# Performance work log

Measured on AMD Instinct MI355X. Metric: run time of the kernel, lower is better.

Reference implementation:

```python
import jax, jax.numpy as jnp
import numpy as np

R = 4
EPS = 0.1


def _box(x, r=R):
    # Depthwise (2r+1)x(2r+1) mean filter with 'SAME' zero padding, faithful to
    # F.conv2d(x, box_kernel, groups=C, padding='same').
    c = x.shape[1]
    k = 2 * r + 1
    kernel = jnp.full((c, 1, k, k), 1.0 / (k * k), dtype=x.dtype)  # OIHW, groups=C
    return jax.lax.conv_general_dilated(
        x, kernel, window_strides=(1, 1), padding='SAME',
        dimension_numbers=('NCHW', 'OIHW', 'NCHW'), feature_group_count=c)


def setup_inputs() -> dict:
    key = jax.random.key(0)
    k1, k2 = jax.random.split(key)
    x = jax.random.uniform(k1, (8, 3, 768, 768), dtype=jnp.float32)
    y = jax.random.uniform(k2, (8, 3, 768, 768), dtype=jnp.float32)
    return {"x": x, "y": y}


def reference(x, y):
    n, c, h, w = x.shape
    # N: box filter of an all-ones [1,1,H,W] image (edge-normalization counts)
    N = _box(jnp.ones((1, 1, h, w), dtype=x.dtype))
    mean_x = _box(x) / N
    mean_y = _box(y) / N
    cov_xy = _box(x * y) / N - mean_x * mean_y
    var_x = _box(x * x) / N - mean_x * mean_x
    A = cov_xy / (var_x + EPS)
    b = mean_y - A * mean_x
    mean_A = _box(A) / N
    mean_b = _box(b) / N
    return mean_A * x + mean_b
```

## Files before the change

### kernel.cpp

```cpp
#include <hip/hip_runtime.h>

#define H 768
#define W 768
#define SW 256
#define RW 272
#define ABWID 264
#define ROWS 64
#define STEPS 80
#define RADIUS 4

__global__ __launch_bounds__(256, 4) void gf_stream(
    const float* __restrict__ xg, const float* __restrict__ yg,
    float* __restrict__ outg)
{
    __shared__ float2 xyrow[RW];
    __shared__ float  xring[9][RW];
    __shared__ float2 abrow[ABWID];
    __shared__ float4 tring[9][8];

    const int t     = threadIdx.x;
    const int strip = blockIdx.x;
    const int band  = blockIdx.y;
    const int plane = blockIdx.z;
    const int base  = strip * SW;
    const int R0    = band * ROWS;

    const float* xp = xg + (size_t)plane * (H * W);
    const float* yp = yg + (size_t)plane * (H * W);
    float*       op = outg + (size_t)plane * (H * W);

    const int  a_abs   = base + t - 4;
    const bool a_colok = (a_abs >= 0) && (a_abs < W);
    const float invCwA = a_colok
        ? 1.0f / (float)(min(a_abs + RADIUS, W - 1) - max(a_abs - RADIUS, 0) + 1) : 0.f;
    const int  a2_abs   = base + 252 + t;
    const bool a2_colok = (t < 8) && (a2_abs < W);
    const float invCwA2 = a2_colok
        ? 1.0f / (float)(min(a2_abs + RADIUS, W - 1) - max(a2_abs - RADIUS, 0) + 1) : 0.f;
    const int   c_abs  = base + t;
    const float invCwO = 1.0f / (float)(min(c_abs + RADIUS, W - 1) - max(c_abs - RADIUS, 0) + 1);
    const int  lc1   = base + t - 8;
    const bool lc1ok = (lc1 >= 0) && (lc1 < W);
    const int  lc2   = base + 248 + t;
    const bool lc2ok = (t < 16) && (lc2 < W);

    float hx[9], hy[9], hxy[9], hxx[9];
    float hA9[9], hB9[9];
#pragma unroll
    for (int i = 0; i < 9; ++i) { hx[i] = hy[i] = hxy[i] = hxx[i] = 0.f; hA9[i] = hB9[i] = 0.f; }
    float vx = 0.f, vy = 0.f, vxy = 0.f, vxx = 0.f;
    float v2x = 0.f, v2y = 0.f, v2xy = 0.f, v2xx = 0.f;
    float vA = 0.f, vB = 0.f;

    if (t < 72) ((float4*)tring)[t] = make_float4(0.f, 0.f, 0.f, 0.f);

    float gx, gy, gx2, gy2;
    {
        int gr = R0 - 8;
        bool rok = (gr >= 0);
        const float* xr = xp + gr * W;
        const float* yr = yp + gr * W;
        gx  = (rok && lc1ok) ? xr[lc1] : 0.f;
        gy  = (rok && lc1ok) ? yr[lc1] : 0.f;
        gx2 = (rok && lc2ok) ? xr[lc2] : 0.f;
        gy2 = (rok && lc2ok) ? yr[lc2] : 0.f;
    }

    for (int so = 0; so < STEPS; so += 9) {
#pragma unroll
        for (int oo = 0; oo < 9; ++oo) {
            const int s = so + oo;
            if (s < STEPS) {
                const int r = R0 - 16 + s;

                __syncthreads();

                const int wr = (r + 8) % 9;
                xyrow[t] = make_float2(gx, gy);
                xring[wr][t] = gx;
                if (t < 16) {
                    xyrow[256 + t] = make_float2(gx2, gy2);
                    xring[wr][256 + t] = gx2;
                }
                {
                    int gr = r + 9;
                    bool rok = (gr >= 0) && (gr < H);
                    const float* xr = xp + gr * W;
                    const float* yr = yp + gr * W;
                    gx  = (rok && lc1ok) ? xr[lc1] : 0.f;
                    gy  = (rok && lc1ok) ? yr[lc1] : 0.f;
                    gx2 = (rok && lc2ok) ? xr[lc2] : 0.f;
                    gy2 = (rok && lc2ok) ? yr[lc2] : 0.f;
                }

                __syncthreads();

                float nx = 0.f, ny = 0.f, nxy = 0.f, nxx = 0.f;
#pragma unroll
                for (int d = 0; d < 9; ++d) {
                    float2 v = xyrow[t + d];
                    nx += v.x; ny += v.y; nxy += v.x * v.y; nxx += v.x * v.x;
                }
                vx  += nx  - hx[oo];  hx[oo]  = nx;
                vy  += ny  - hy[oo];  hy[oo]  = ny;
                vxy += nxy - hxy[oo]; hxy[oo] = nxy;
                vxx += nxx - hxx[oo]; hxx[oo] = nxx;

                const int ra = r + 4;
                const bool rowok = (s >= 8) && (ra >= 0) && (ra < H);
                const float invChA = rowok
                    ? 1.0f / (float)(min(ra + RADIUS, H - 1) - max(ra - RADIUS, 0) + 1) : 0.f;
                float Aout = 0.f, Bout = 0.f;
                if (rowok && a_colok) {
                    float invN = invChA * invCwA;
                    float mx = vx * invN, my = vy * invN;
                    float cov = vxy * invN - mx * my;
                    float vr  = vxx * invN - mx * mx;
                    Aout = cov / (vr + 0.1f);
                    Bout = my - Aout * mx;
                }
                abrow[t] = make_float2(Aout, Bout);

                if (t < 8) {
                    float ex = 0.f, ey = 0.f, exy = 0.f, exx = 0.f;
#pragma unroll
                    for (int d = 0; d < 9; ++d) {
                        float2 v = xyrow[256 + t + d];
                        ex += v.x; ey += v.y; exy += v.x * v.y; exx += v.x * v.x;
                    }
                    float4 old = tring[oo][t];
                    v2x += ex - old.x; v2y += ey - old.y;
                    v2xy += exy - old.z; v2xx += exx - old.w;
                    tring[oo][t] = make_float4(ex, ey, exy, exx);
                    float A2 = 0.f, B2 = 0.f;
                    if (rowok && a2_colok) {
                        float invN = invChA * invCwA2;
                        float mx = v2x * invN, my = v2y * invN;
                        float cov = v2xy * invN - mx * my;
                        float vr  = v2xx * invN - mx * mx;
                        A2 = cov / (vr + 0.1f);
                        B2 = my - A2 * mx;
                    }
                    abrow[256 + t] = make_float2(A2, B2);
                }

                __syncthreads();

                float hAn = 0.f, hBn = 0.f;
#pragma unroll
                for (int d = 0; d < 9; ++d) {
                    float2 v = abrow[t + d];
                    hAn += v.x; hBn += v.y;
                }
                vA += hAn - hA9[oo]; hA9[oo] = hAn;
                vB += hBn - hB9[oo]; hB9[oo] = hBn;

                if (s >= 16) {
                    float xo = xring[r % 9][t + 8];
                    const float invChO =
                        1.0f / (float)(min(r + RADIUS, H - 1) - max(r - RADIUS, 0) + 1);
                    float invN2 = invChO * invCwO;
                    op[r * W + c_abs] = (vA * invN2) * xo + (vB * invN2);
                }
            }
        }
    }
}

extern "C" void kernel_launch(void* const* d_in, const int* in_sizes, int n_in,
                              void* d_out, int out_size, void* d_ws, size_t ws_size,
                              hipStream_t stream) {
    const float* x = (const float*)d_in[0];
    const float* y = (const float*)d_in[1];
    float* out = (float*)d_out;

    dim3 grid(W / SW, H / ROWS, 24);
    dim3 block(256);
    hipLaunchKernelGGL(gf_stream, grid, block, 0, stream, x, y, out);
}
```

Before: 107.5 us.

## Process two rows per step with double-buffered LDS to cut barriers

Restructures the streaming loop to handle two rows per iteration, with double-buffered row and A/B buffers in shared memory. This drops from three barriers per row to one barrier per two rows. The x value for the output is now reloaded from global memory instead of an LDS ring, and the division is replaced by a hardware reciprocal approximation. The trade-offs are more registers, extra global reads, and slightly lower precision from rcp.

```diff
diff --git a/kernel.cpp b/kernel.cpp
--- a/kernel.cpp
+++ b/kernel.cpp
@@ -4,26 +4,23 @@
 #define W 768
 #define SW 256
 #define RW 272
-#define ABWID 264
+#define ABW 264
 #define ROWS 64
-#define STEPS 80
+#define NSTEP 40
 #define RADIUS 4
 
-__global__ __launch_bounds__(256, 4) void gf_stream(
+__global__ __launch_bounds__(256, 4) void gf_stream2(
     const float* __restrict__ xg, const float* __restrict__ yg,
     float* __restrict__ outg)
 {
-    __shared__ float2 xyrow[RW];
-    __shared__ float  xring[9][RW];
-    __shared__ float2 abrow[ABWID];
+    __shared__ float2 xybuf[2][2][RW];
+    __shared__ float2 abbuf[2][2][ABW];
     __shared__ float4 tring[9][8];
 
     const int t     = threadIdx.x;
-    const int strip = blockIdx.x;
-    const int band  = blockIdx.y;
+    const int base  = blockIdx.x * SW;
+    const int R0    = blockIdx.y * ROWS;
     const int plane = blockIdx.z;
-    const int base  = strip * SW;
-    const int R0    = band * ROWS;
 
     const float* xp = xg + (size_t)plane * (H * W);
     const float* yp = yg + (size_t)plane * (H * W);
@@ -47,120 +44,195 @@
     float hx[9], hy[9], hxy[9], hxx[9];
     float hA9[9], hB9[9];
 #pragma unroll
-    for (int i = 0; i < 9; ++i) { hx[i] = hy[i] = hxy[i] = hxx[i] = 0.f; hA9[i] = hB9[i] = 0.f; }
-    float vx = 0.f, vy = 0.f, vxy = 0.f, vxx = 0.f;
-    float v2x = 0.f, v2y = 0.f, v2xy = 0.f, v2xx = 0.f;
-    float vA = 0.f, vB = 0.f;
-
-    if (t < 72) ((float4*)tring)[t] = make_float4(0.f, 0.f, 0.f, 0.f);
-
-    float gx, gy, gx2, gy2;
+    for (int i = 0; i < 9; ++i) { hx[i]=hy[i]=hxy[i]=hxx[i]=0.f; hA9[i]=hB9[i]=0.f; }
+    float vx=0.f, vy=0.f, vxy=0.f, vxx=0.f;
+    float v2x=0.f, v2y=0.f, v2xy=0.f, v2xx=0.f;
+    float vA=0.f, vB=0.f;
+
+    if (t < 72) ((float4*)tring)[t] = make_float4(0.f,0.f,0.f,0.f);
+
     {
-        int gr = R0 - 8;
-        bool rok = (gr >= 0);
-        const float* xr = xp + gr * W;
-        const float* yr = yp + gr * W;
-        gx  = (rok && lc1ok) ? xr[lc1] : 0.f;
-        gy  = (rok && lc1ok) ? yr[lc1] : 0.f;
-        gx2 = (rok && lc2ok) ? xr[lc2] : 0.f;
-        gy2 = (rok && lc2ok) ? yr[lc2] : 0.f;
+        int g0 = R0 - 8, g1 = R0 - 7;
+        bool k0 = (g0 >= 0), k1 = (g1 >= 0);
+        const float *x0 = xp + g0 * W, *y0 = yp + g0 * W;
+        const float *x1 = xp + g1 * W, *y1 = yp + g1 * W;
+        float a, b;
+        a = (k0 && lc1ok) ? x0[lc1] : 0.f;  b = (k0 && lc1ok) ? y0[lc1] : 0.f;
+        xybuf[0][0][t] = make_float2(a, b);
+        a = (k1 && lc1ok) ? x1[lc1] : 0.f;  b = (k1 && lc1ok) ? y1[lc1] : 0.f;
+        xybuf[0][1][t] = make_float2(a, b);
+        if (t < 16) {
+            a = (k0 && lc2ok) ? x0[lc2] : 0.f;  b = (k0 && lc2ok) ? y0[lc2] : 0.f;
+            xybuf[0][0][256 + t] = make_float2(a, b);
+            a = (k1 && lc2ok) ? x1[lc2] : 0.f;  b = (k1 && lc2ok) ? y1[lc2] : 0.f;
+            xybuf[0][1][256 + t] = make_float2(a, b);
+        }
     }
-
-    for (int so = 0; so < STEPS; so += 9) {
-#pragma unroll
-        for (int oo = 0; oo < 9; ++oo) {
-            const int s = so + oo;
-            if (s < STEPS) {
-                const int r = R0 - 16 + s;
+    float p0x, p0y, p0x2, p0y2, p1x, p1y, p1x2, p1y2;
+    {
+        int g0 = R0 - 6, g1 = R0 - 5;
+        bool k0 = (g0 >= 0), k1 = (g1 >= 0);
+        const float *x0 = xp + g0 * W, *y0 = yp + g0 * W;
+        const float *x1 = xp + g1 * W, *y1 = yp + g1 * W;
+        p0x  = (k0 && lc1ok) ? x0[lc1] : 0.f;  p0y  = (k0 && lc1ok) ? y0[lc1] : 0.f;
+        p1x  = (k1 && lc1ok) ? x1[lc1] : 0.f;  p1y  = (k1 && lc1ok) ? y1[lc1] : 0.f;
+        p0x2 = (k0 && lc2ok) ? x0[lc2] : 0.f;  p0y2 = (k0 && lc2ok) ? y0[lc2] : 0.f;
+        p1x2 = (k1 && lc2ok) ? x1[lc2] : 0.f;  p1y2 = (k1 && lc2ok) ? y1[lc2] : 0.f;
+    }
+    __syncthreads();
+
+    for (int S0 = 0; S0 < NSTEP; S0 += 9) {
+#pragma unroll
+        for (int u = 0; u < 9; ++u) {
+            const int S = S0 + u;
+            if (S < NSTEP) {
+                const int r0  = R0 - 16 + 2 * S;
+                const int cur = S & 1, nxt = cur ^ 1;
+
+                xybuf[nxt][0][t] = make_float2(p0x, p0y);
+                xybuf[nxt][1][t] = make_float2(p1x, p1y);
+                if (t < 16) {
+                    xybuf[nxt][0][256 + t] = make_float2(p0x2, p0y2);
+                    xybuf[nxt][1][256 + t] = make_float2(p1x2, p1y2);
+                }
+                {
+                    int g0 = r0 + 12, g1 = r0 + 13;
+                    bool k0 = (g0 >= 0) && (g0 < H);
+                    bool k1 = (g1 >= 0) && (g1 < H);
+                    const float *x0 = xp + g0 * W, *y0 = yp + g0 * W;
+                    const float *x1 = xp + g1 * W, *y1 = yp + g1 * W;
+                    p0x  = (k0 && lc1ok) ? x0[lc1] : 0.f;  p0y  = (k0 && lc1ok) ? y0[lc1] : 0.f;
+                    p1x  = (k1 && lc1ok) ? x1[lc1] : 0.f;  p1y  = (k1 && lc1ok) ? y1[lc1] : 0.f;
+                    p0x2 = (k0 && lc2ok) ? x0[lc2] : 0.f;  p0y2 = (k0 && lc2ok) ? y0[lc2] : 0.f;
+                    p1x2 = (k1 && lc2ok) ? x1[lc2] : 0.f;  p1y2 = (k1 && lc2ok) ? y1[lc2] : 0.f;
+                }
+                float xq0 = (r0 >= 0)     ? xp[r0 * W + c_abs]       : 0.f;
+                float xq1 = (r0 + 1 >= 0) ? xp[(r0 + 1) * W + c_abs] : 0.f;
+
+                {
+                    const int sl = (2 * u) % 9;
+                    float nx=0.f, ny=0.f, nxy=0.f, nxx=0.f;
+#pragma unroll
+                    for (int d = 0; d < 9; ++d) {
+                        float2 v = xybuf[cur][0][t + d];
+                        nx += v.x; ny += v.y; nxy += v.x * v.y; nxx += v.x * v.x;
+                    }
+                    vx  += nx  - hx[sl];  hx[sl]  = nx;
+                    vy  += ny  - hy[sl];  hy[sl]  = ny;
+                    vxy += nxy - hxy[sl]; hxy[sl] = nxy;
+                    vxx += nxx - hxx[sl]; hxx[sl] = nxx;
+
+                    const int ra = r0 + 4;
+                    const bool rowok = (S >= 4) && (ra >= 0) && (ra < H);
+                    float Aout = 0.f, Bout = 0.f;
+                    if (rowok && a_colok) {
+                        const float invCh = 1.0f /
+                            (float)(min(ra + RADIUS, H - 1) - max(ra - RADIUS, 0) + 1);
+                        float invN = invCh * invCwA;
+                        float mx = vx * invN, my = vy * invN;
+                        float cov = vxy * invN - mx * my;
+                        float vr  = vxx * invN - mx * mx;
+                        float Ai = cov * __builtin_amdgcn_rcpf(vr + 0.1f);
+                        Aout = Ai; Bout = my - Ai * mx;
+                    }
+                    abbuf[cur][0][t] = make_float2(Aout, Bout);
+                }
+                {
+                    const int sl = (2 * u + 1) % 9;
+                    float nx=0.f, ny=0.f, nxy=0.f, nxx=0.f;
+#pragma unroll
+                    for (int d = 0; d < 9; ++d) {
+                        float2 v = xybuf[cur][1][t + d];
+                        nx += v.x; ny += v.y; nxy += v.x * v.y; nxx += v.x * v.x;
+                    }
+                    vx  += nx  - hx[sl];  hx[sl]  = nx;
+                    vy  += ny  - hy[sl];  hy[sl]  = ny;
+                    vxy += nxy - hxy[sl]; hxy[sl] = nxy;
+                    vxx += nxx - hxx[sl]; hxx[sl] = nxx;
+
+                    const int ra = r0 + 5;
+                    const bool rowok = (S >= 4) && (ra >= 0) && (ra < H);
+                    float Aout = 0.f, Bout = 0.f;
+                    if (rowok && a_colok) {
+                        const float invCh = 1.0f /
+                            (float)(min(ra + RADIUS, H - 1) - max(ra - RADIUS, 0) + 1);
+                        float invN = invCh * invCwA;
+                        float mx = vx * invN, my = vy * invN;
+                        float cov = vxy * invN - mx * my;
+                        float vr  = vxx * invN - mx * mx;
+                        float Ai = cov * __builtin_amdgcn_rcpf(vr + 0.1f);
+                        Aout = Ai; Bout = my - Ai * mx;
+                    }
+                    abbuf[cur][1][t] = make_float2(Aout, Bout);
+                }
+                if (t < 8) {
+#pragma unroll
+                    for (int j = 0; j < 2; ++j) {
+                        const int sl = (2 * u + j) % 9;
+                        float ex=0.f, ey=0.f, exy=0.f, exx=0.f;
+#pragma unroll
+                        for (int d = 0; d < 9; ++d) {
+                            float2 v = xybuf[cur][j][256 + t + d];
+                            ex += v.x; ey += v.y; exy += v.x * v.y; exx += v.x * v.x;
+                        }
+                        float4 old = tring[sl][t];
+                        v2x += ex - old.x; v2y += ey - old.y;
+                        v2xy += exy - old.z; v2xx += exx - old.w;
+                        tring[sl][t] = make_float4(ex, ey, exy, exx);
+
+                        const int ra = r0 + 4 + j;
+                        const bool rowok = (S >= 4) && (ra >= 0) && (ra < H);
+                        float A2 = 0.f, B2 = 0.f;
+                        if (rowok && a2_colok) {
+                            const float invCh = 1.0f /
+                                (float)(min(ra + RADIUS, H - 1) - max(ra - RADIUS, 0) + 1);
+                            float invN = invCh * invCwA2;
+                            float mx = v2x * invN, my = v2y * invN;
+                            float cov = v2xy * invN - mx * my;
+                            float vr  = v2xx * invN - mx * mx;
+                            float Ai = cov * __builtin_amdgcn_rcpf(vr + 0.1f);
+                            A2 = Ai; B2 = my - Ai * mx;
+                        }
+                        abbuf[cur][j][256 + t] = make_float2(A2, B2);
+                    }
+                }
 
                 __syncthreads();
 
-                const int wr = (r + 8) % 9;
-                xyrow[t] = make_float2(gx, gy);
-                xring[wr][t] = gx;
-                if (t < 16) {
-                    xyrow[256 + t] = make_float2(gx2, gy2);
-                    xring[wr][256 + t] = gx2;
-                }
-                {
-                    int gr = r + 9;
-                    bool rok = (gr >= 0) && (gr < H);
-                    const float* xr = xp + gr * W;
-                    const float* yr = yp + gr * W;
-                    gx  = (rok && lc1ok) ? xr[lc1] : 0.f;
-                    gy  = (rok && lc1ok) ? yr[lc1] : 0.f;
-                    gx2 = (rok && lc2ok) ? xr[lc2] : 0.f;
-                    gy2 = (rok && lc2ok) ? yr[lc2] : 0.f;
-                }
-
-                __syncthreads();
-
-                float nx = 0.f, ny = 0.f, nxy = 0.f, nxx = 0.f;
-#pragma unroll
-                for (int d = 0; d < 9; ++d) {
-                    float2 v = xyrow[t + d];
-                    nx += v.x; ny += v.y; nxy += v.x * v.y; nxx += v.x * v.x;
-                }
-                vx  += nx  - hx[oo];  hx[oo]  = nx;
-                vy  += ny  - hy[oo];  hy[oo]  = ny;
-                vxy += nxy - hxy[oo]; hxy[oo] = nxy;
-                vxx += nxx - hxx[oo]; hxx[oo] = nxx;
-
-                const int ra = r + 4;
-                const bool rowok = (s >= 8) && (ra >= 0) && (ra < H);
-                const float invChA = rowok
-                    ? 1.0f / (float)(min(ra + RADIUS, H - 1) - max(ra - RADIUS, 0) + 1) : 0.f;
-                float Aout = 0.f, Bout = 0.f;
-                if (rowok && a_colok) {
-                    float invN = invChA * invCwA;
-                    float mx = vx * invN, my = vy * invN;
-                    float cov = vxy * invN - mx * my;
-                    float vr  = vxx * invN - mx * mx;
-                    Aout = cov / (vr + 0.1f);
-                    Bout = my - Aout * mx;
-                }
-                abrow[t] = make_float2(Aout, Bout);
-
-                if (t < 8) {
-                    float ex = 0.f, ey = 0.f, exy = 0.f, exx = 0.f;
-#pragma unroll
-                    for (int d = 0; d < 9; ++d) {
-                        float2 v = xyrow[256 + t + d];
-                        ex += v.x; ey += v.y; exy += v.x * v.y; exx += v.x * v.x;
-                    }
-                    float4 old = tring[oo][t];
-                    v2x += ex - old.x; v2y += ey - old.y;
-                    v2xy += exy - old.z; v2xx += exx - old.w;
-                    tring[oo][t] = make_float4(ex, ey, exy, exx);
-                    float A2 = 0.f, B2 = 0.f;
-                    if (rowok && a2_colok) {
-                        float invN = invChA * invCwA2;
-                        float mx = v2x * invN, my = v2y * invN;
-                        float cov = v2xy * invN - mx * my;
-                        float vr  = v2xx * invN - mx * mx;
-                        A2 = cov / (vr + 0.1f);
-                        B2 = my - A2 * mx;
-                    }
-                    abrow[256 + t] = make_float2(A2, B2);
-                }
-
-                __syncthreads();
-
-                float hAn = 0.f, hBn = 0.f;
-#pragma unroll
-                for (int d = 0; d < 9; ++d) {
-                    float2 v = abrow[t + d];
-                    hAn += v.x; hBn += v.y;
-                }
-                vA += hAn - hA9[oo]; hA9[oo] = hAn;
-                vB += hBn - hB9[oo]; hB9[oo] = hBn;
-
-                if (s >= 16) {
-                    float xo = xring[r % 9][t + 8];
-                    const float invChO =
-                        1.0f / (float)(min(r + RADIUS, H - 1) - max(r - RADIUS, 0) + 1);
-                    float invN2 = invChO * invCwO;
-                    op[r * W + c_abs] = (vA * invN2) * xo + (vB * invN2);
+                {
+                    const int sl = (2 * u) % 9;
+                    float hA=0.f, hB=0.f;
+#pragma unroll
+                    for (int d = 0; d < 9; ++d) {
+                        float2 v = abbuf[cur][0][t + d];
+                        hA += v.x; hB += v.y;
+                    }
+                    vA += hA - hA9[sl]; hA9[sl] = hA;
+                    vB += hB - hB9[sl]; hB9[sl] = hB;
+                    if (S >= 8) {
+                        const float invCh = 1.0f /
+                            (float)(min(r0 + RADIUS, H - 1) - max(r0 - RADIUS, 0) + 1);
+                        float invN = invCh * invCwO;
+                        op[r0 * W + c_abs] = (vA * invN) * xq0 + (vB * invN);
+                    }
+                }
+                {
+                    const int sl = (2 * u + 1) % 9;
+                    float hA=0.f, hB=0.f;
+#pragma unroll
+                    for (int d = 0; d < 9; ++d) {
+                        float2 v = abbuf[cur][1][t + d];
+                        hA += v.x; hB += v.y;
+                    }
+                    vA += hA - hA9[sl]; hA9[sl] = hA;
+                    vB += hB - hB9[sl]; hB9[sl] = hB;
+                    if (S >= 8) {
+                        const int r = r0 + 1;
+                        const float invCh = 1.0f /
+                            (float)(min(r + RADIUS, H - 1) - max(r - RADIUS, 0) + 1);
+                        float invN = invCh * invCwO;
+                        op[r * W + c_abs] = (vA * invN) * xq1 + (vB * invN);
+                    }
                 }
             }
         }
@@ -176,5 +248,5 @@
 
     dim3 grid(W / SW, H / ROWS, 24);
     dim3 block(256);
-    hipLaunchKernelGGL(gf_stream, grid, block, 0, stream, x, y, out);
+    hipLaunchKernelGGL(gf_stream2, grid, block, 0, stream, x, y, out);
 }
```

Result: faster. 103.8 us (-3.4%).

## Double-buffer row stages to cut barriers to one per row, shrink row bands

Applied to the files above, without the earlier changes.

Double-buffers the xy row and AB row shared arrays so each streamed row needs one __syncthreads instead of three. Input loads are prefetched one extra row ahead, and the x ring grows to 11 slots to cover the longer lag. The band height drops from 64 to 48 rows, which gives more blocks but a higher share of warm-up rows (16 of 64 steps instead of 16 of 80). The divides become fast reciprocals, which slightly changes the precision of A.

```diff
diff --git a/kernel.cpp b/kernel.cpp
--- a/kernel.cpp
+++ b/kernel.cpp
@@ -4,26 +4,25 @@
 #define W 768
 #define SW 256
 #define RW 272
-#define ABWID 264
-#define ROWS 64
-#define STEPS 80
+#define ABW 264
+#define ROWS 48
+#define STEPS 64
+#define XR 11
 #define RADIUS 4
 
-__global__ __launch_bounds__(256, 4) void gf_stream(
+__global__ __launch_bounds__(256, 4) void gf_stream6(
     const float* __restrict__ xg, const float* __restrict__ yg,
     float* __restrict__ outg)
 {
-    __shared__ float2 xyrow[RW];
-    __shared__ float  xring[9][RW];
-    __shared__ float2 abrow[ABWID];
+    __shared__ float2 xybuf[2][RW];
+    __shared__ float2 abbuf[2][ABW];
+    __shared__ float  xring[XR][RW];
     __shared__ float4 tring[9][8];
 
     const int t     = threadIdx.x;
-    const int strip = blockIdx.x;
-    const int band  = blockIdx.y;
+    const int base  = blockIdx.x * SW;
+    const int R0    = blockIdx.y * ROWS;
     const int plane = blockIdx.z;
-    const int base  = strip * SW;
-    const int R0    = band * ROWS;
 
     const float* xp = xg + (size_t)plane * (H * W);
     const float* yp = yg + (size_t)plane * (H * W);
@@ -45,122 +44,132 @@
     const bool lc2ok = (t < 16) && (lc2 < W);
 
     float hx[9], hy[9], hxy[9], hxx[9];
-    float hA9[9], hB9[9];
+    float aA[9], aB[9];
 #pragma unroll
-    for (int i = 0; i < 9; ++i) { hx[i] = hy[i] = hxy[i] = hxx[i] = 0.f; hA9[i] = hB9[i] = 0.f; }
-    float vx = 0.f, vy = 0.f, vxy = 0.f, vxx = 0.f;
-    float v2x = 0.f, v2y = 0.f, v2xy = 0.f, v2xx = 0.f;
-    float vA = 0.f, vB = 0.f;
+    for (int i = 0; i < 9; ++i) { hx[i]=hy[i]=hxy[i]=hxx[i]=0.f; aA[i]=aB[i]=0.f; }
+    float vx=0.f, vy=0.f, vxy=0.f, vxx=0.f;
+    float v2x=0.f, v2y=0.f, v2xy=0.f, v2xx=0.f;
+    float vA=0.f, vB=0.f;
 
-    if (t < 72) ((float4*)tring)[t] = make_float4(0.f, 0.f, 0.f, 0.f);
+    if (t < 72) ((float4*)tring)[t] = make_float4(0.f,0.f,0.f,0.f);
 
-    float gx, gy, gx2, gy2;
     {
-        int gr = R0 - 8;
-        bool rok = (gr >= 0);
-        const float* xr = xp + gr * W;
-        const float* yr = yp + gr * W;
-        gx  = (rok && lc1ok) ? xr[lc1] : 0.f;
-        gy  = (rok && lc1ok) ? yr[lc1] : 0.f;
-        gx2 = (rok && lc2ok) ? xr[lc2] : 0.f;
-        gy2 = (rok && lc2ok) ? yr[lc2] : 0.f;
+        int g = R0 - 8;
+        bool k = (g >= 0);
+        const float *xr_ = xp + g * W, *yr_ = yp + g * W;
+        float a = (k && lc1ok) ? xr_[lc1] : 0.f;
+        float b = (k && lc1ok) ? yr_[lc1] : 0.f;
+        xybuf[0][t] = make_float2(a, b);
+        if (t < 16) {
+            float c = (k && lc2ok) ? xr_[lc2] : 0.f;
+            float d = (k && lc2ok) ? yr_[lc2] : 0.f;
+            xybuf[0][256 + t] = make_float2(c, d);
+        }
     }
+    float px_, py_, px2_, py2_;
+    {
+        int g = R0 - 7;
+        bool k = (g >= 0);
+        const float *xr_ = xp + g * W, *yr_ = yp + g * W;
+        px_  = (k && lc1ok) ? xr_[lc1] : 0.f;  py_  = (k && lc1ok) ? yr_[lc1] : 0.f;
+        px2_ = (k && lc2ok) ? xr_[lc2] : 0.f;  py2_ = (k && lc2ok) ? yr_[lc2] : 0.f;
+    }
+    __syncthreads();
 
-    for (int so = 0; so < STEPS; so += 9) {
+    for (int S0 = 0; S0 < STEPS; S0 += 9) {
 #pragma unroll
-        for (int oo = 0; oo < 9; ++oo) {
-            const int s = so + oo;
-            if (s < STEPS) {
-                const int r = R0 - 16 + s;
+        for (int u = 0; u < 9; ++u) {
+            const int S = S0 + u;
+            if (S < STEPS) {
+                const int r   = R0 - 16 + S;
+                const int cur = S & 1, nxt = cur ^ 1;
+                const int slw = (R0 + S + 15) % XR;
+                const int slr = (R0 + S + 6)  % XR;
 
-                __syncthreads();
-
-                const int wr = (r + 8) % 9;
-                xyrow[t] = make_float2(gx, gy);
-                xring[wr][t] = gx;
+                xybuf[nxt][t] = make_float2(px_, py_);
+                xring[slw][t] = px_;
                 if (t < 16) {
-                    xyrow[256 + t] = make_float2(gx2, gy2);
-                    xring[wr][256 + t] = gx2;
+                    xybuf[nxt][256 + t] = make_float2(px2_, py2_);
+                    xring[slw][256 + t] = px2_;
                 }
                 {
-                    int gr = r + 9;
-                    bool rok = (gr >= 0) && (gr < H);
-                    const float* xr = xp + gr * W;
-                    const float* yr = yp + gr * W;
-                    gx  = (rok && lc1ok) ? xr[lc1] : 0.f;
-                    gy  = (rok && lc1ok) ? yr[lc1] : 0.f;
-                    gx2 = (rok && lc2ok) ? xr[lc2] : 0.f;
-                    gy2 = (rok && lc2ok) ? yr[lc2] : 0.f;
+                    int g = r + 10;
+                    bool k = (g >= 0) && (g < H);
+                    const float *xr_ = xp + g * W, *yr_ = yp + g * W;
+                    px_  = (k && lc1ok) ? xr_[lc1] : 0.f;  py_  = (k && lc1ok) ? yr_[lc1] : 0.f;
+                    px2_ = (k && lc2ok) ? xr_[lc2] : 0.f;  py2_ = (k && lc2ok) ? yr_[lc2] : 0.f;
+                }
+
+                float nx=0.f, ny=0.f, nxy=0.f, nxx=0.f;
+#pragma unroll
+                for (int d = 0; d < 9; ++d) {
+                    float2 v = xybuf[cur][t + d];
+                    nx += v.x; ny += v.y; nxy += v.x * v.y; nxx += v.x * v.x;
+                }
+                vx  += nx  - hx[u];  hx[u]  = nx;
+                vy  += ny  - hy[u];  hy[u]  = ny;
+                vxy += nxy - hxy[u]; hxy[u] = nxy;
+                vxx += nxx - hxx[u]; hxx[u] = nxx;
+
+                const int ra = r + 4;
+                if (S >= 8) {
+                    float A0 = 0.f, B0 = 0.f;
+                    if (a_colok && ra >= 0 && ra < H) {
+                        const float invCh = 1.0f /
+                            (float)(min(ra + RADIUS, H - 1) - max(ra - RADIUS, 0) + 1);
+                        float invN = invCh * invCwA;
+                        float mx = vx * invN, my = vy * invN;
+                        float cov = vxy * invN - mx * my;
+                        float vr  = vxx * invN - mx * mx;
+                        A0 = cov * __builtin_amdgcn_rcpf(vr + 0.1f);
+                        B0 = my - A0 * mx;
+                    }
+                    abbuf[cur][t] = make_float2(A0, B0);
+                }
+                if (t < 8) {
+                    float ex=0.f, ey=0.f, exy=0.f, exx=0.f;
+#pragma unroll
+                    for (int d = 0; d < 9; ++d) {
+                        float2 v = xybuf[cur][256 + t + d];
+                        ex += v.x; ey += v.y; exy += v.x * v.y; exx += v.x * v.x;
+                    }
+                    float4 o = tring[u][t];
+                    v2x += ex - o.x; v2y += ey - o.y; v2xy += exy - o.z; v2xx += exx - o.w;
+                    tring[u][t] = make_float4(ex, ey, exy, exx);
+                    if (S >= 8) {
+                        float A2 = 0.f, B2 = 0.f;
+                        if (a2_colok && ra >= 0 && ra < H) {
+                            const float invCh = 1.0f /
+                                (float)(min(ra + RADIUS, H - 1) - max(ra - RADIUS, 0) + 1);
+                            float invN = invCh * invCwA2;
+                            float mx = v2x * invN, my = v2y * invN;
+                            float cov = v2xy * invN - mx * my;
+                            float vr  = v2xx * invN - mx * mx;
+                            A2 = cov * __builtin_amdgcn_rcpf(vr + 0.1f);
+                            B2 = my - A2 * mx;
+                        }
+                        abbuf[cur][256 + t] = make_float2(A2, B2);
+                    }
                 }
 
                 __syncthreads();
 
-                float nx = 0.f, ny = 0.f, nxy = 0.f, nxx = 0.f;
-#pragma unroll
-                for (int d = 0; d < 9; ++d) {
-                    float2 v = xyrow[t + d];
-                    nx += v.x; ny += v.y; nxy += v.x * v.y; nxx += v.x * v.x;
-                }
-                vx  += nx  - hx[oo];  hx[oo]  = nx;
-                vy  += ny  - hy[oo];  hy[oo]  = ny;
-                vxy += nxy - hxy[oo]; hxy[oo] = nxy;
-                vxx += nxx - hxx[oo]; hxx[oo] = nxx;
-
-                const int ra = r + 4;
-                const bool rowok = (s >= 8) && (ra >= 0) && (ra < H);
-                const float invChA = rowok
-                    ? 1.0f / (float)(min(ra + RADIUS, H - 1) - max(ra - RADIUS, 0) + 1) : 0.f;
-                float Aout = 0.f, Bout = 0.f;
-                if (rowok && a_colok) {
-                    float invN = invChA * invCwA;
-                    float mx = vx * invN, my = vy * invN;
-                    float cov = vxy * invN - mx * my;
-                    float vr  = vxx * invN - mx * mx;
-                    Aout = cov / (vr + 0.1f);
-                    Bout = my - Aout * mx;
-                }
-                abrow[t] = make_float2(Aout, Bout);
-
-                if (t < 8) {
-                    float ex = 0.f, ey = 0.f, exy = 0.f, exx = 0.f;
+                if (S >= 8) {
+                    float hA=0.f, hB=0.f;
 #pragma unroll
                     for (int d = 0; d < 9; ++d) {
-                        float2 v = xyrow[256 + t + d];
-                        ex += v.x; ey += v.y; exy += v.x * v.y; exx += v.x * v.x;
+                        float2 v = abbuf[cur][t + d];
+                        hA += v.x; hB += v.y;
                     }
-                    float4 old = tring[oo][t];
-                    v2x += ex - old.x; v2y += ey - old.y;
-                    v2xy += exy - old.z; v2xx += exx - old.w;
-                    tring[oo][t] = make_float4(ex, ey, exy, exx);
-                    float A2 = 0.f, B2 = 0.f;
-                    if (rowok && a2_colok) {
-                        float invN = invChA * invCwA2;
-                        float mx = v2x * invN, my = v2y * invN;
-                        float cov = v2xy * invN - mx * my;
-                        float vr  = v2xx * invN - mx * mx;
-                        A2 = cov / (vr + 0.1f);
-                        B2 = my - A2 * mx;
+                    vA += hA - aA[u]; aA[u] = hA;
+                    vB += hB - aB[u]; aB[u] = hB;
+                    if (S >= 16) {
+                        float xo = xring[slr][t + 8];
+                        const float invCh = 1.0f /
+                            (float)(min(r + RADIUS, H - 1) - max(r - RADIUS, 0) + 1);
+                        float invN = invCh * invCwO;
+                        op[r * W + c_abs] = (vA * invN) * xo + (vB * invN);
                     }
-                    abrow[256 + t] = make_float2(A2, B2);
-                }
-
-                __syncthreads();
-
-                float hAn = 0.f, hBn = 0.f;
-#pragma unroll
-                for (int d = 0; d < 9; ++d) {
-                    float2 v = abrow[t + d];
-                    hAn += v.x; hBn += v.y;
-                }
-                vA += hAn - hA9[oo]; hA9[oo] = hAn;
-                vB += hBn - hB9[oo]; hB9[oo] = hBn;
-
-                if (s >= 16) {
-                    float xo = xring[r % 9][t + 8];
-                    const float invChO =
-                        1.0f / (float)(min(r + RADIUS, H - 1) - max(r - RADIUS, 0) + 1);
-                    float invN2 = invChO * invCwO;
-                    op[r * W + c_abs] = (vA * invN2) * xo + (vB * invN2);
                 }
             }
         }
@@ -176,5 +185,5 @@
 
     dim3 grid(W / SW, H / ROWS, 24);
     dim3 block(256);
-    hipLaunchKernelGGL(gf_stream, grid, block, 0, stream, x, y, out);
+    hipLaunchKernelGGL(gf_stream6, grid, block, 0, stream, x, y, out);
 }
```

Measured after the change: 123.9 us. +15.2%, slower.
